# Kernel optimization log

Hardware: AMD Instinct MI355X
Metric: run time of the kernel (lower is better)

The kernel has to match this reference:

```python
import jax, jax.numpy as jnp
import numpy as np

B, S, D_MODEL, D_FF = 4, 2048, 1024, 4096


def setup_inputs() -> dict:
    key = jax.random.key(0)
    ks = jax.random.split(key, 8)
    return {
        "x": jax.random.normal(ks[0], (B, S, D_MODEL), dtype=jnp.float32),
        "W1": jax.random.normal(ks[1], (D_MODEL, D_FF), dtype=jnp.float32) * (1.0 / np.sqrt(D_MODEL)),
        "b1": jnp.zeros((D_FF,), dtype=jnp.float32),
        "quantum_phases": jax.random.normal(ks[2], (D_FF,), dtype=jnp.float32) * (2.0 * np.pi),
        "quantum_weights_real": jax.random.normal(ks[3], (D_FF,), dtype=jnp.float32) * 0.1,
        "quantum_weights_imag": jax.random.normal(ks[4], (D_FF,), dtype=jnp.float32) * 0.1,
        "W2": jax.random.normal(ks[5], (D_FF, D_MODEL), dtype=jnp.float32) * (1.0 / np.sqrt(D_FF)),
        "b2": jnp.zeros((D_MODEL,), dtype=jnp.float32),
    }


def _quantum_transform(hidden, theta, w_real, w_imag):
    # hidden: [B,S,d_ff]; theta/w_real/w_imag: [d_ff] broadcast over channels
    imag = w_imag * jnp.sin(theta + hidden * 0.1)
    quantum_phase = jnp.cos(theta) * w_real + jnp.sin(theta) * w_imag  # [d_ff]
    return hidden + quantum_phase * imag * 0.1


def reference(x, W1, b1, quantum_phases, quantum_weights_real, quantum_weights_imag, W2, b2):
    hidden = jnp.einsum("bsd,df->bsf", x, W1) + b1  # [B,S,d_ff]
    q = _quantum_transform(hidden, quantum_phases, quantum_weights_real, quantum_weights_imag)
    act = jax.nn.relu(q)  # dropout is identity in eval mode
    return jnp.einsum("bsf,fd->bsd", act, W2) + b2
```

## Files before the change

### kernel.cpp

```cpp
#include <hip/hip_runtime.h>

typedef __bf16 bf16x8 __attribute__((ext_vector_type(8)));
typedef short  s16x8  __attribute__((ext_vector_type(8)));
typedef float  f32x4  __attribute__((ext_vector_type(4)));

#define DEVINL __device__ __forceinline__

DEVINL unsigned short f2bf(float f) {
  unsigned int u = __builtin_bit_cast(unsigned int, f);
  u += 0x7fffu + ((u >> 16) & 1u);
  return (unsigned short)(u >> 16);
}

DEVINL void async16(const void* g, void* l) {
  __builtin_amdgcn_global_load_lds(
      (const __attribute__((address_space(1))) unsigned int*)g,
      (__attribute__((address_space(3))) unsigned int*)l, 16, 0, 0);
}


__global__ __launch_bounds__(256) void prep(
    const float* __restrict__ x, const float* __restrict__ W1,
    const float* __restrict__ W2, const float* __restrict__ theta,
    const float* __restrict__ wre, const float* __restrict__ wim,
    unsigned short* __restrict__ xb, unsigned short* __restrict__ w1t,
    unsigned short* __restrict__ w2t, float* __restrict__ c1) {
  __shared__ unsigned short tile[32][33];
  const int b = blockIdx.x;
  const int tid = threadIdx.x;
  if (b < 1024) {
    int i = b * 256 + tid;
#pragma unroll
    for (int k = 0; k < 8; ++k, i += 262144) {
      float4 v = ((const float4*)x)[i];
      ushort4 o;
      o.x = f2bf(v.x); o.y = f2bf(v.y); o.z = f2bf(v.z); o.w = f2bf(v.w);
      ((ushort4*)xb)[i] = o;
    }
  } else if (b < 5120) {
    int bb = b - 1024;
    int bc = (bb & 127) * 32, br = (bb >> 7) * 32;
    int tx = tid & 31, ty = tid >> 5;
#pragma unroll
    for (int i = 0; i < 32; i += 8)
      tile[ty + i][tx] = f2bf(W1[(size_t)(br + ty + i) * 4096 + (bc + tx)]);
    __syncthreads();
#pragma unroll
    for (int i = 0; i < 32; i += 8)
      w1t[(size_t)(bc + ty + i) * 1024 + (br + tx)] = tile[tx][ty + i];
  } else if (b < 9216) {
    int bb = b - 5120;
    int bc = (bb & 31) * 32, br = (bb >> 5) * 32;
    int tx = tid & 31, ty = tid >> 5;
#pragma unroll
    for (int i = 0; i < 32; i += 8)
      tile[ty + i][tx] = f2bf(W2[(size_t)(br + ty + i) * 1024 + (bc + tx)]);
    __syncthreads();
#pragma unroll
    for (int i = 0; i < 32; i += 8)
      w2t[(size_t)(bc + ty + i) * 4096 + (br + tx)] = tile[tx][ty + i];
  } else {
    int i = (b - 9216) * 256 + tid;
    float t = theta[i];
    c1[i] = (cosf(t) * wre[i] + sinf(t) * wim[i]) * wim[i] * 0.1f;
  }
}


__global__ __launch_bounds__(512, 1) void gemm1k(
    const unsigned short* __restrict__ A,
    const unsigned short* __restrict__ Bt,
    const float* __restrict__ bias,
    const float* __restrict__ theta,
    const float* __restrict__ c1,
    unsigned short* __restrict__ Cout) {
  constexpr int K = 1024, N = 4096, NT = 16, REPS = 2;
  constexpr int WROWS = 128, M_REP = 8, MH = 4;
  constexpr int ABYTES = 32768, AH = 16384, AL = 2;
  constexpr int BUFSZ = 65536;
  constexpr int nTilesN = 8;

  __shared__ __align__(16) char lds[2 * BUFSZ + 16384];

  int nwg = gridDim.x;
  int wg = blockIdx.x;
  int sw = (wg & 7) * (nwg >> 3) + (wg >> 3);
  int rowBase = (sw / nTilesN) * 256;
  int colBase = (sw % nTilesN) * 512;

  const int t = threadIdx.x;
  const int lane = t & 63;
  const int wid = t >> 6;
  const int wr = wid >> 2, wc = wid & 3;
  const int lr = lane & 15;
  const int lg = lane >> 4;
  const int r7 = lane & 7;

  const int srow = t >> 3;
  const int scolB = ((t & 7) * 16) ^ ((srow & 7) << 4);
  const unsigned short* aSrcB = A  + (size_t)(rowBase + srow) * K + (scolB >> 1);
  const unsigned short* bSrcB = Bt + (size_t)(colBase + srow) * K + (scolB >> 1);

  const int aRd = (wr * WROWS + lr) * 128 + ((lg ^ r7) << 4);
  const int bRd = ABYTES + (wc * 64 + lr) * 128 + ((lg ^ r7) << 4);

#define STAGE_AU(S, U, P) do {                                              \
    _Pragma("unroll") for (int j = 0; j < AL; ++j)                          \
      async16(aSrcB + ((size_t)((U) * WROWS + j * 64) * K + (size_t)(S) * 64),\
              &lds[(P) * BUFSZ + (U) * AH + j * 8192 + t * 16]);            \
  } while (0)
#define STAGE_BU(SRC, S, U, P) do {                                         \
    _Pragma("unroll") for (int j = 0; j < 2; ++j)                           \
      async16((SRC) + ((size_t)((U) * 128 + j * 64) * K + (size_t)(S) * 64),\
              &lds[(P) * BUFSZ + ABYTES + (U) * 16384 + j * 8192 + t * 16]);\
  } while (0)
#define LOAD_A(MHh, P)                                                      \
  _Pragma("unroll") for (int mi = 0; mi < MH; ++mi)                         \
  _Pragma("unroll") for (int ks = 0; ks < 2; ++ks)                          \
    a[mi][ks] = __builtin_bit_cast(bf16x8, *(const s16x8*)&lds[             \
        (P) * BUFSZ + ((aRd + ((MHh) * MH + mi) * 2048) ^ (ks << 6))])
#define LOAD_B(NHh, P)                                                      \
  _Pragma("unroll") for (int nn = 0; nn < 2; ++nn)                          \
  _Pragma("unroll") for (int ks = 0; ks < 2; ++ks)                          \
    b[(NHh) * 2 + nn][ks] = __builtin_bit_cast(bf16x8, *(const s16x8*)&lds[ \
        (P) * BUFSZ + ((bRd + ((NHh) * 2 + nn) * 2048) ^ (ks << 6))])
#define QUAD(MHh, NHh)                                                      \
  __builtin_amdgcn_s_setprio(1);                                            \
  _Pragma("unroll") for (int mi = 0; mi < MH; ++mi)                         \
  _Pragma("unroll") for (int nn = 0; nn < 2; ++nn)                          \
  _Pragma("unroll") for (int ks = 0; ks < 2; ++ks)                          \
    acc[(MHh) * MH + mi][(NHh) * 2 + nn] =                                  \
        __builtin_amdgcn_mfma_f32_16x16x32_bf16(                            \
            a[mi][ks], b[(NHh) * 2 + nn][ks],                               \
            acc[(MHh) * MH + mi][(NHh) * 2 + nn], 0, 0, 0);                 \
  __builtin_amdgcn_s_setprio(0)
#define BAR() __builtin_amdgcn_s_barrier()
#define LG0() asm volatile("s_waitcnt lgkmcnt(0)" ::: "memory")
#define WIN(T, P) do {                                                      \
                                                                \
    LOAD_A(0, P); LOAD_B(0, P);                                             \
    if ((T) + 1 < NT) {                                                     \
      STAGE_AU((T) + 1, 0, (P) ^ 1);                                        \
      STAGE_AU((T) + 1, 1, (P) ^ 1);                                        \
    }                                                                       \
    QUAD(0, 0);                                                             \
    LOAD_B(1, P);                                                           \
    QUAD(0, 1);                                                             \
    LG0(); BAR();                                                           \
                                                                \
    LOAD_A(1, P);                                                           \
    if ((T) + 2 < NT) {                                                     \
      STAGE_BU(bSrcR, (T) + 2, 0, P);                                       \
      STAGE_BU(bSrcR, (T) + 2, 1, P);                                       \
    }                                                                       \
    QUAD(1, 0);                                                             \
    QUAD(1, 1);                                                             \
    LG0();                                                                  \
    if ((T) < NT - 2) {                                                     \
      asm volatile("s_waitcnt vmcnt(4)" ::: "memory");                      \
    } else if ((T) == NT - 2) {                                             \
      asm volatile("s_waitcnt vmcnt(0)" ::: "memory");                      \
    }                                                                       \
    BAR();                                                                  \
  } while (0)

  STAGE_AU(0, 0, 0); STAGE_AU(0, 1, 0);
  STAGE_BU(bSrcB, 0, 0, 0); STAGE_BU(bSrcB, 0, 1, 0);
  STAGE_BU(bSrcB, 1, 0, 1); STAGE_BU(bSrcB, 1, 1, 1);
  asm volatile("s_waitcnt vmcnt(4)" ::: "memory");
  BAR();

  for (int rep = 0; rep < REPS; ++rep) {
    const unsigned short* bSrcR = bSrcB + (size_t)rep * 256 * K;
    f32x4 acc[M_REP][4] = {};
    bf16x8 a[MH][2], b[4][2];

    for (int T = 0; T < NT; T += 2) {
      WIN(T, 0);
      WIN(T + 1, 1);
    }

    if (rep + 1 < REPS) {
      const unsigned short* bSrcN = bSrcB + (size_t)(rep + 1) * 256 * K;
      STAGE_AU(0, 0, 0); STAGE_AU(0, 1, 0);
      STAGE_BU(bSrcN, 0, 0, 0); STAGE_BU(bSrcN, 0, 1, 0);
      STAGE_BU(bSrcN, 1, 0, 1); STAGE_BU(bSrcN, 1, 1, 1);
    }

    const int colR = colBase + rep * 256;
    const int ocol0 = colR + wc * 64 + lr;
    float bvv[4], thv[4], ccv[4];
#pragma unroll
    for (int ni = 0; ni < 4; ++ni) {
      int n = ocol0 + ni * 16;
      bvv[ni] = bias[n]; thv[ni] = theta[n]; ccv[ni] = c1[n];
    }
    const int SB = 2 * BUFSZ + wid * 2048;
    const size_t growB = (size_t)(rowBase + wr * WROWS) * N;
    const int rd = lane >> 3;
    const int bo = (lane & 7) * 16;
#pragma unroll
    for (int mi = 0; mi < M_REP; ++mi) {
#pragma unroll
      for (int ni = 0; ni < 4; ++ni) {
#pragma unroll
        for (int r = 0; r < 4; ++r) {
          int row16 = lg * 4 + r;
          float h = acc[mi][ni][r] + bvv[ni];
          float q = h + ccv[ni] * __sinf(thv[ni] + 0.1f * h);
          unsigned short v = f2bf(fmaxf(q, 0.f));
          int ad = SB + row16 * 128 +
                   (((ni * 16 + lr) * 2) ^ ((row16 & 7) << 4));
          *(unsigned short*)&lds[ad] = v;
        }
      }
      s16x8 w0 = *(const s16x8*)&lds[SB + rd * 128 + (bo ^ ((rd & 7) << 4))];
      s16x8 w1 = *(const s16x8*)&lds[SB + (rd + 8) * 128 +
                                     (bo ^ ((rd & 7) << 4))];
      unsigned short* dst = Cout + growB + (size_t)(mi * 16 + rd) * N +
                            colR + wc * 64 + (lane & 7) * 8;
      *(s16x8*)dst = w0;
      *(s16x8*)(dst + (size_t)8 * N) = w1;
    }

    if (rep + 1 < REPS) {
      asm volatile("s_waitcnt vmcnt(16)" ::: "memory");
      BAR();
    }
  }
#undef WIN
#undef QUAD
#undef LOAD_A
#undef LOAD_B
#undef STAGE_AU
#undef STAGE_BU
#undef BAR
#undef LG0
}


__global__ __launch_bounds__(512, 1) void gemm2k(
    const unsigned short* __restrict__ A,
    const unsigned short* __restrict__ Bt,
    const float* __restrict__ bias,
    float* __restrict__ Cout) {
  constexpr int K = 4096, N = 1024, NT = 64;
  constexpr int WROWS = 64, M_REP = 4, MH = 2;
  constexpr int ABYTES = 16384, AH = 8192, AL = 1;
  constexpr int BUFSZ = 49152;
  constexpr int nTilesN = 4;

  __shared__ __align__(16) char lds[2 * BUFSZ + 32768];

  int nwg = gridDim.x;
  int wg = blockIdx.x;
  int sw = (wg & 7) * (nwg >> 3) + (wg >> 3);
  int rowBase = (sw / nTilesN) * 128;
  int colBase = (sw % nTilesN) * 256;

  const int t = threadIdx.x;
  const int lane = t & 63;
  const int wid = t >> 6;
  const int wr = wid >> 2, wc = wid & 3;
  const int lr = lane & 15;
  const int lg = lane >> 4;
  const int r7 = lane & 7;

  const int srow = t >> 3;
  const int scolB = ((t & 7) * 16) ^ ((srow & 7) << 4);
  const unsigned short* aSrcB = A  + (size_t)(rowBase + srow) * K + (scolB >> 1);
  const unsigned short* bSrcB = Bt + (size_t)(colBase + srow) * K + (scolB >> 1);

  const int aRd = (wr * WROWS + lr) * 128 + ((lg ^ r7) << 4);
  const int bRd = ABYTES + (wc * 64 + lr) * 128 + ((lg ^ r7) << 4);

  f32x4 acc[M_REP][4] = {};
  bf16x8 a[MH][2], b[4][2];

#define STAGE_AU(S, U, P)                                                   \
  async16(aSrcB + ((size_t)((U) * 64) * K + (size_t)(S) * 64),              \
          &lds[(P) * BUFSZ + (U) * AH + t * 16])
#define STAGE_BU(S, U, P) do {                                              \
    _Pragma("unroll") for (int j = 0; j < 2; ++j)                           \
      async16(bSrcB + ((size_t)((U) * 128 + j * 64) * K + (size_t)(S) * 64),\
              &lds[(P) * BUFSZ + ABYTES + (U) * 16384 + j * 8192 + t * 16]);\
  } while (0)
#define LOAD_A(MHh, P)                                                      \
  _Pragma("unroll") for (int mi = 0; mi < MH; ++mi)                         \
  _Pragma("unroll") for (int ks = 0; ks < 2; ++ks)                          \
    a[mi][ks] = __builtin_bit_cast(bf16x8, *(const s16x8*)&lds[             \
        (P) * BUFSZ + ((aRd + ((MHh) * MH + mi) * 2048) ^ (ks << 6))])
#define LOAD_B(NHh, P)                                                      \
  _Pragma("unroll") for (int nn = 0; nn < 2; ++nn)                          \
  _Pragma("unroll") for (int ks = 0; ks < 2; ++ks)                          \
    b[(NHh) * 2 + nn][ks] = __builtin_bit_cast(bf16x8, *(const s16x8*)&lds[ \
        (P) * BUFSZ + ((bRd + ((NHh) * 2 + nn) * 2048) ^ (ks << 6))])
#define QUAD(MHh, NHh)                                                      \
  __builtin_amdgcn_s_setprio(1);                                            \
  _Pragma("unroll") for (int mi = 0; mi < MH; ++mi)                         \
  _Pragma("unroll") for (int nn = 0; nn < 2; ++nn)                          \
  _Pragma("unroll") for (int ks = 0; ks < 2; ++ks)                          \
    acc[(MHh) * MH + mi][(NHh) * 2 + nn] =                                  \
        __builtin_amdgcn_mfma_f32_16x16x32_bf16(                            \
            a[mi][ks], b[(NHh) * 2 + nn][ks],                               \
            acc[(MHh) * MH + mi][(NHh) * 2 + nn], 0, 0, 0);                 \
  __builtin_amdgcn_s_setprio(0)
#define BAR() __builtin_amdgcn_s_barrier()
#define LG0() asm volatile("s_waitcnt lgkmcnt(0)" ::: "memory")
#define WIN(T, P) do {                                                      \
                                                                \
    LOAD_A(0, P); LOAD_B(0, P);                                             \
    if ((T) + 1 < NT) {                                                     \
      STAGE_AU((T) + 1, 0, (P) ^ 1);                                        \
      STAGE_AU((T) + 1, 1, (P) ^ 1);                                        \
    }                                                                       \
    QUAD(0, 0);                                                             \
    LOAD_B(1, P);                                                           \
    QUAD(0, 1);                                                             \
    LG0(); BAR();                                                           \
                                                                \
    LOAD_A(1, P);                                                           \
    if ((T) + 2 < NT) {                                                     \
      STAGE_BU((T) + 2, 0, P);                                              \
      STAGE_BU((T) + 2, 1, P);                                              \
    }                                                                       \
    QUAD(1, 0);                                                             \
    QUAD(1, 1);                                                             \
    LG0();                                                                  \
    if ((T) < NT - 2) {                                                     \
      asm volatile("s_waitcnt vmcnt(4)" ::: "memory");                      \
    } else if ((T) == NT - 2) {                                             \
      asm volatile("s_waitcnt vmcnt(0)" ::: "memory");                      \
    }                                                                       \
    BAR();                                                                  \
  } while (0)

  STAGE_AU(0, 0, 0); STAGE_AU(0, 1, 0);
  STAGE_BU(0, 0, 0); STAGE_BU(0, 1, 0);
  STAGE_BU(1, 0, 1); STAGE_BU(1, 1, 1);
  asm volatile("s_waitcnt vmcnt(4)" ::: "memory");
  BAR();

  for (int T = 0; T < NT; T += 2) {
    WIN(T, 0);
    WIN(T + 1, 1);
  }
#undef WIN
#undef QUAD
#undef LOAD_A
#undef LOAD_B
#undef STAGE_AU
#undef STAGE_BU
#undef BAR

  const int ocol0 = colBase + wc * 64 + lr;
  float bvv[4];
#pragma unroll
  for (int ni = 0; ni < 4; ++ni) bvv[ni] = bias[ocol0 + ni * 16];
  const int SB = 2 * BUFSZ + wid * 4096;
  const int orowB = rowBase + wr * WROWS;
  const int rd = lane >> 3;
  const int bo = (lane & 7) * 16;
#pragma unroll
  for (int mi = 0; mi < M_REP; ++mi) {
#pragma unroll
    for (int ni = 0; ni < 4; ++ni) {
#pragma unroll
      for (int r = 0; r < 4; ++r) {
        int row16 = lg * 4 + r;
        int ad = SB + row16 * 256 +
                 (((ni * 16 + lr) * 4) ^ ((row16 & 7) << 4));
        *(float*)&lds[ad] = acc[mi][ni][r] + bvv[ni];
      }
    }
    asm volatile("s_waitcnt lgkmcnt(0)" ::: "memory");
    f32x4 v00 = *(const f32x4*)&lds[SB + rd * 256 + (bo ^ ((rd & 7) << 4))];
    f32x4 v01 = *(const f32x4*)&lds[SB + rd * 256 +
                                    ((bo + 128) ^ ((rd & 7) << 4))];
    f32x4 v10 = *(const f32x4*)&lds[SB + (rd + 8) * 256 +
                                    (bo ^ ((rd & 7) << 4))];
    f32x4 v11 = *(const f32x4*)&lds[SB + (rd + 8) * 256 +
                                    ((bo + 128) ^ ((rd & 7) << 4))];
    float* dst0 = Cout + (size_t)(orowB + mi * 16 + rd) * N +
                  colBase + wc * 64 + (lane & 7) * 4;
    *(f32x4*)dst0 = v00;
    *(f32x4*)(dst0 + 32) = v01;
    float* dst1 = dst0 + (size_t)8 * N;
    *(f32x4*)dst1 = v10;
    *(f32x4*)(dst1 + 32) = v11;
    asm volatile("s_waitcnt lgkmcnt(0)" ::: "memory");
  }
#undef LG0
}


extern "C" void kernel_launch(void* const* d_in, const int* in_sizes, int n_in,
                              void* d_out, int out_size, void* d_ws,
                              size_t ws_size, hipStream_t stream) {
  const float* x     = (const float*)d_in[0];
  const float* W1    = (const float*)d_in[1];
  const float* b1    = (const float*)d_in[2];
  const float* theta = (const float*)d_in[3];
  const float* qwr   = (const float*)d_in[4];
  const float* qwi   = (const float*)d_in[5];
  const float* W2    = (const float*)d_in[6];
  const float* b2    = (const float*)d_in[7];
  float* out = (float*)d_out;

  const int DF = 4096;
  size_t need = ((size_t)96 << 20) + DF * sizeof(float);
  if (ws_size < need) return;

  char* ws = (char*)d_ws;
  unsigned short* xb   = (unsigned short*)ws;
  unsigned short* w1t  = (unsigned short*)(ws + ((size_t)16 << 20));
  unsigned short* w2t  = (unsigned short*)(ws + ((size_t)24 << 20));
  unsigned short* actb = (unsigned short*)(ws + ((size_t)32 << 20));
  float* c1 = (float*)(ws + ((size_t)96 << 20));

  prep<<<9232, 256, 0, stream>>>(x, W1, W2, theta, qwr, qwi,
                                 xb, w1t, w2t, c1);
  gemm1k<<<256, 512, 0, stream>>>(xb, w1t, b1, theta, c1, actb);
  gemm2k<<<256, 512, 0, stream>>>(actb, w2t, b2, out);
}
```

Before: 146.6 us.

## Shrink gemm1 tiles to 128x256 with triple-buffered LDS and 1024 workgroups

Gemm1 now uses 128x256 output tiles instead of 256x512 processed in two reps, and launches 1024 workgroups rather than 256. The K loop moves from double to triple buffering, with A and B staged two steps ahead. This is meant to improve load balance and wave count across CUs and to deepen the prefetch. In exchange each tile has lower arithmetic intensity, so more global and L2 traffic is needed per output element.

After: 161.5 us. 1.1x slower.

```diff
diff --git a/kernel.cpp b/kernel.cpp
--- a/kernel.cpp
+++ b/kernel.cpp
@@ -74,19 +74,18 @@
     const float* __restrict__ theta,
     const float* __restrict__ c1,
     unsigned short* __restrict__ Cout) {
-  constexpr int K = 1024, N = 4096, NT = 16, REPS = 2;
-  constexpr int WROWS = 128, M_REP = 8, MH = 4;
-  constexpr int ABYTES = 32768, AH = 16384, AL = 2;
-  constexpr int BUFSZ = 65536;
-  constexpr int nTilesN = 8;
-
-  __shared__ __align__(16) char lds[2 * BUFSZ + 16384];
+  constexpr int K = 1024, N = 4096, NT = 16;
+  constexpr int ABYTES = 16384, AH = 8192;
+  constexpr int BUFSZ = 49152;
+  constexpr int nTilesN = 16;
+
+  __shared__ __align__(16) char lds[3 * BUFSZ];
 
   int nwg = gridDim.x;
   int wg = blockIdx.x;
   int sw = (wg & 7) * (nwg >> 3) + (wg >> 3);
-  int rowBase = (sw / nTilesN) * 256;
-  int colBase = (sw % nTilesN) * 512;
+  int rowBase = (sw / nTilesN) * 128;
+  int colBase = (sw % nTilesN) * 256;
 
   const int t = threadIdx.x;
   const int lane = t & 63;
@@ -101,24 +100,27 @@
   const unsigned short* aSrcB = A  + (size_t)(rowBase + srow) * K + (scolB >> 1);
   const unsigned short* bSrcB = Bt + (size_t)(colBase + srow) * K + (scolB >> 1);
 
-  const int aRd = (wr * WROWS + lr) * 128 + ((lg ^ r7) << 4);
+  const int aRd = (wr * 64 + lr) * 128 + ((lg ^ r7) << 4);
   const int bRd = ABYTES + (wc * 64 + lr) * 128 + ((lg ^ r7) << 4);
 
-#define STAGE_AU(S, U, P) do {                                              \
-    _Pragma("unroll") for (int j = 0; j < AL; ++j)                          \
-      async16(aSrcB + ((size_t)((U) * WROWS + j * 64) * K + (size_t)(S) * 64),\
-              &lds[(P) * BUFSZ + (U) * AH + j * 8192 + t * 16]);            \
+  f32x4 acc[4][4] = {};
+  bf16x8 a[2][2], b[4][2];
+
+#define STAGE_A(S, P) do {                                                  \
+    async16(aSrcB + (size_t)(S) * 64, &lds[(P) * BUFSZ + t * 16]);          \
+    async16(aSrcB + ((size_t)64 * K + (size_t)(S) * 64),                    \
+            &lds[(P) * BUFSZ + AH + t * 16]);                               \
   } while (0)
-#define STAGE_BU(SRC, S, U, P) do {                                         \
-    _Pragma("unroll") for (int j = 0; j < 2; ++j)                           \
-      async16((SRC) + ((size_t)((U) * 128 + j * 64) * K + (size_t)(S) * 64),\
-              &lds[(P) * BUFSZ + ABYTES + (U) * 16384 + j * 8192 + t * 16]);\
+#define STAGE_B(S, P) do {                                                  \
+    _Pragma("unroll") for (int u = 0; u < 4; ++u)                           \
+      async16(bSrcB + ((size_t)(u * 64) * K + (size_t)(S) * 64),            \
+              &lds[(P) * BUFSZ + ABYTES + u * 8192 + t * 16]);              \
   } while (0)
 #define LOAD_A(MHh, P)                                                      \
-  _Pragma("unroll") for (int mi = 0; mi < MH; ++mi)                         \
+  _Pragma("unroll") for (int mi = 0; mi < 2; ++mi)                          \
   _Pragma("unroll") for (int ks = 0; ks < 2; ++ks)                          \
     a[mi][ks] = __builtin_bit_cast(bf16x8, *(const s16x8*)&lds[             \
-        (P) * BUFSZ + ((aRd + ((MHh) * MH + mi) * 2048) ^ (ks << 6))])
+        (P) * BUFSZ + ((aRd + ((MHh) * 2 + mi) * 2048) ^ (ks << 6))])
 #define LOAD_B(NHh, P)                                                      \
   _Pragma("unroll") for (int nn = 0; nn < 2; ++nn)                          \
   _Pragma("unroll") for (int ks = 0; ks < 2; ++ks)                          \
@@ -126,116 +128,93 @@
         (P) * BUFSZ + ((bRd + ((NHh) * 2 + nn) * 2048) ^ (ks << 6))])
 #define QUAD(MHh, NHh)                                                      \
   __builtin_amdgcn_s_setprio(1);                                            \
-  _Pragma("unroll") for (int mi = 0; mi < MH; ++mi)                         \
+  _Pragma("unroll") for (int mi = 0; mi < 2; ++mi)                          \
   _Pragma("unroll") for (int nn = 0; nn < 2; ++nn)                          \
   _Pragma("unroll") for (int ks = 0; ks < 2; ++ks)                          \
-    acc[(MHh) * MH + mi][(NHh) * 2 + nn] =                                  \
+    acc[(MHh) * 2 + mi][(NHh) * 2 + nn] =                                   \
         __builtin_amdgcn_mfma_f32_16x16x32_bf16(                            \
             a[mi][ks], b[(NHh) * 2 + nn][ks],                               \
-            acc[(MHh) * MH + mi][(NHh) * 2 + nn], 0, 0, 0);                 \
+            acc[(MHh) * 2 + mi][(NHh) * 2 + nn], 0, 0, 0);                  \
   __builtin_amdgcn_s_setprio(0)
 #define BAR() __builtin_amdgcn_s_barrier()
 #define LG0() asm volatile("s_waitcnt lgkmcnt(0)" ::: "memory")
-#define WIN(T, P) do {                                                      \
+#define WIN(T, P, PN) do {                                                  \
                                                                 \
     LOAD_A(0, P); LOAD_B(0, P);                                             \
-    if ((T) + 1 < NT) {                                                     \
-      STAGE_AU((T) + 1, 0, (P) ^ 1);                                        \
-      STAGE_AU((T) + 1, 1, (P) ^ 1);                                        \
-    }                                                                       \
+    if ((T) + 2 < NT) STAGE_A((T) + 2, PN);                                 \
     QUAD(0, 0);                                                             \
     LOAD_B(1, P);                                                           \
     QUAD(0, 1);                                                             \
     LG0(); BAR();                                                           \
                                                                 \
     LOAD_A(1, P);                                                           \
-    if ((T) + 2 < NT) {                                                     \
-      STAGE_BU(bSrcR, (T) + 2, 0, P);                                       \
-      STAGE_BU(bSrcR, (T) + 2, 1, P);                                       \
-    }                                                                       \
+    if ((T) + 2 < NT) STAGE_B((T) + 2, PN);                                 \
     QUAD(1, 0);                                                             \
     QUAD(1, 1);                                                             \
     LG0();                                                                  \
-    if ((T) < NT - 2) {                                                     \
-      asm volatile("s_waitcnt vmcnt(4)" ::: "memory");                      \
-    } else if ((T) == NT - 2) {                                             \
+    if ((T) + 2 < NT) {                                                     \
+      asm volatile("s_waitcnt vmcnt(6)" ::: "memory");                      \
+    } else if ((T) + 1 < NT) {                                              \
       asm volatile("s_waitcnt vmcnt(0)" ::: "memory");                      \
     }                                                                       \
     BAR();                                                                  \
   } while (0)
 
-  STAGE_AU(0, 0, 0); STAGE_AU(0, 1, 0);
-  STAGE_BU(bSrcB, 0, 0, 0); STAGE_BU(bSrcB, 0, 1, 0);
-  STAGE_BU(bSrcB, 1, 0, 1); STAGE_BU(bSrcB, 1, 1, 1);
-  asm volatile("s_waitcnt vmcnt(4)" ::: "memory");
+  STAGE_A(0, 0); STAGE_B(0, 0);
+  STAGE_A(1, 1); STAGE_B(1, 1);
+  asm volatile("s_waitcnt vmcnt(6)" ::: "memory");
   BAR();
 
-  for (int rep = 0; rep < REPS; ++rep) {
-    const unsigned short* bSrcR = bSrcB + (size_t)rep * 256 * K;
-    f32x4 acc[M_REP][4] = {};
-    bf16x8 a[MH][2], b[4][2];
-
-    for (int T = 0; T < NT; T += 2) {
-      WIN(T, 0);
-      WIN(T + 1, 1);
-    }
-
-    if (rep + 1 < REPS) {
-      const unsigned short* bSrcN = bSrcB + (size_t)(rep + 1) * 256 * K;
-      STAGE_AU(0, 0, 0); STAGE_AU(0, 1, 0);
-      STAGE_BU(bSrcN, 0, 0, 0); STAGE_BU(bSrcN, 0, 1, 0);
-      STAGE_BU(bSrcN, 1, 0, 1); STAGE_BU(bSrcN, 1, 1, 1);
-    }
-
-    const int colR = colBase + rep * 256;
-    const int ocol0 = colR + wc * 64 + lr;
-    float bvv[4], thv[4], ccv[4];
-#pragma unroll
-    for (int ni = 0; ni < 4; ++ni) {
-      int n = ocol0 + ni * 16;
-      bvv[ni] = bias[n]; thv[ni] = theta[n]; ccv[ni] = c1[n];
-    }
-    const int SB = 2 * BUFSZ + wid * 2048;
-    const size_t growB = (size_t)(rowBase + wr * WROWS) * N;
-    const int rd = lane >> 3;
-    const int bo = (lane & 7) * 16;
-#pragma unroll
-    for (int mi = 0; mi < M_REP; ++mi) {
-#pragma unroll
-      for (int ni = 0; ni < 4; ++ni) {
-#pragma unroll
-        for (int r = 0; r < 4; ++r) {
-          int row16 = lg * 4 + r;
-          float h = acc[mi][ni][r] + bvv[ni];
-          float q = h + ccv[ni] * __sinf(thv[ni] + 0.1f * h);
-          unsigned short v = f2bf(fmaxf(q, 0.f));
-          int ad = SB + row16 * 128 +
-                   (((ni * 16 + lr) * 2) ^ ((row16 & 7) << 4));
-          *(unsigned short*)&lds[ad] = v;
-        }
-      }
-      s16x8 w0 = *(const s16x8*)&lds[SB + rd * 128 + (bo ^ ((rd & 7) << 4))];
-      s16x8 w1 = *(const s16x8*)&lds[SB + (rd + 8) * 128 +
-                                     (bo ^ ((rd & 7) << 4))];
-      unsigned short* dst = Cout + growB + (size_t)(mi * 16 + rd) * N +
-                            colR + wc * 64 + (lane & 7) * 8;
-      *(s16x8*)dst = w0;
-      *(s16x8*)(dst + (size_t)8 * N) = w1;
-    }
-
-    if (rep + 1 < REPS) {
-      asm volatile("s_waitcnt vmcnt(16)" ::: "memory");
-      BAR();
-    }
-  }
+  for (int T = 0; T < NT - 1; T += 3) {
+    WIN(T, 0, 2);
+    WIN(T + 1, 1, 0);
+    WIN(T + 2, 2, 1);
+  }
+  WIN(NT - 1, 0, 2);
+
 #undef WIN
 #undef QUAD
 #undef LOAD_A
 #undef LOAD_B
-#undef STAGE_AU
-#undef STAGE_BU
+#undef STAGE_A
+#undef STAGE_B
 #undef BAR
 #undef LG0
+
+  const int ocol0 = colBase + wc * 64 + lr;
+  float bvv[4], thv[4], ccv[4];
+#pragma unroll
+  for (int ni = 0; ni < 4; ++ni) {
+    int n = ocol0 + ni * 16;
+    bvv[ni] = bias[n]; thv[ni] = theta[n]; ccv[ni] = c1[n];
+  }
+  const int SB = wid * 2048;
+  const size_t growB = (size_t)(rowBase + wr * 64) * N;
+  const int rd = lane >> 3;
+  const int bo = (lane & 7) * 16;
+#pragma unroll
+  for (int mi = 0; mi < 4; ++mi) {
+#pragma unroll
+    for (int ni = 0; ni < 4; ++ni) {
+#pragma unroll
+      for (int r = 0; r < 4; ++r) {
+        int row16 = lg * 4 + r;
+        float h = acc[mi][ni][r] + bvv[ni];
+        float q = h + ccv[ni] * __sinf(thv[ni] + 0.1f * h);
+        unsigned short v = f2bf(fmaxf(q, 0.f));
+        int ad = SB + row16 * 128 +
+                 (((ni * 16 + lr) * 2) ^ ((row16 & 7) << 4));
+        *(unsigned short*)&lds[ad] = v;
+      }
+    }
+    s16x8 w0 = *(const s16x8*)&lds[SB + rd * 128 + (bo ^ ((rd & 7) << 4))];
+    s16x8 w1 = *(const s16x8*)&lds[SB + (rd + 8) * 128 +
+                                   (bo ^ ((rd & 7) << 4))];
+    unsigned short* dst = Cout + growB + (size_t)(mi * 16 + rd) * N +
+                          colBase + wc * 64 + (lane & 7) * 8;
+    *(s16x8*)dst = w0;
+    *(s16x8*)(dst + (size_t)8 * N) = w1;
+  }
 }
 
 
@@ -420,6 +399,6 @@
 
   prep<<<9232, 256, 0, stream>>>(x, W1, W2, theta, qwr, qwi,
                                  xb, w1t, w2t, c1);
-  gemm1k<<<256, 512, 0, stream>>>(xb, w1t, b1, theta, c1, actb);
+  gemm1k<<<1024, 512, 0, stream>>>(xb, w1t, b1, theta, c1, actb);
   gemm2k<<<256, 512, 0, stream>>>(actb, w2t, b2, out);
 }
```
